# Kernel optimization log

Measured on AMD Instinct MI355X. Metric: run time of the kernel, lower is better.

Reference implementation:

```python
import jax, jax.numpy as jnp
import numpy as np

N_NODES = 50000
N_EDGES = 800000
IN_DIM = 128
HID = 128
OUT_DIM = 2


def setup_inputs() -> dict:
    key = jax.random.key(0)
    ks = jax.random.split(key, 10)
    s_in = 1.0 / np.sqrt(IN_DIM)
    s_cat = 1.0 / np.sqrt(2 * HID)
    s_h = 1.0 / np.sqrt(HID)
    return {
        "x": jax.random.normal(ks[0], (N_NODES, IN_DIM), dtype=jnp.float32),
        "edge_index": jax.random.randint(ks[1], (2, N_EDGES), 0, N_NODES, dtype=jnp.int64),
        "W_in": jax.random.uniform(ks[2], (IN_DIM, HID), jnp.float32, -s_in, s_in),
        "b_in": jnp.zeros((HID,), jnp.float32),
        "W1": jax.random.uniform(ks[3], (2 * HID, HID), jnp.float32, -s_cat, s_cat),
        "b1": jnp.zeros((HID,), jnp.float32),
        "W2": jax.random.uniform(ks[4], (HID, HID), jnp.float32, -s_h, s_h),
        "b2": jnp.zeros((HID,), jnp.float32),
        "Wc": jax.random.uniform(ks[5], (HID, OUT_DIM), jnp.float32, -s_h, s_h),
        "bc": jnp.zeros((OUT_DIM,), jnp.float32),
    }


def reference(x, edge_index, W_in, b_in, W1, b1, W2, b2, Wc, bc):
    # Input projection (eval mode: dropout is identity)
    h = jax.nn.relu(x @ W_in + b_in)                      # [N, H]
    src, dst = edge_index[0], edge_index[1]               # PyG: x_j = x[src], x_i = x[dst]
    # Per-edge message: MLP(h_i || h_j). Split the first Linear over the concat
    # halves to avoid materializing the [E, 2H] concat buffer.
    m = h[dst] @ W1[:HID] + h[src] @ W1[HID:] + b1        # [E, H]
    m = jax.nn.relu(m) @ W2 + b2                          # [E, H]
    # Scatter-add aggregation into destination nodes
    h2 = jax.ops.segment_sum(m, dst, num_segments=N_NODES)  # [N, H]
    h2 = jax.nn.relu(h2)
    return h2 @ Wc + bc                                   # [N, OUT]
```

## Files before the change

kernel.cpp:

```cpp
#include <hip/hip_runtime.h>
#include <hip/hip_bf16.h>
#include <hip/hip_fp16.h>

#define N_NODES 50000
#define N_EDGES 800000
#define HID 128
#define NPROJ 391
#define CAP 48
#define OVF_MAX 8192
#define NBIN 196
#define BINSH 8
#define BINCAP 4608
#define NCOARSE 98

typedef __bf16 bf16x8 __attribute__((ext_vector_type(8)));
typedef float f32x4 __attribute__((ext_vector_type(4)));

__global__ __launch_bounds__(256) void prep_kernel(
    const float* __restrict__ Win, const float* __restrict__ W1,
    const float* __restrict__ W2, __bf16* __restrict__ Wsw,
    int* __restrict__ curz)
{
    int id = blockIdx.x * 256 + threadIdx.x;
    int m     = id >> 14;
    int rem   = id & 16383;
    int j     = rem & 7;
    int lane  = (rem >> 3) & 63;
    int ntile = (rem >> 9) & 7;
    int kstep = rem >> 12;
    int k = kstep * 32 + (lane >> 4) * 8 + j;
    int n = ntile * 16 + (lane & 15);
    float v;
    if (m == 0)      v = Win[k * HID + n];
    else if (m == 1) v = W1[k * HID + n];
    else if (m == 2) v = W1[(k + HID) * HID + n];
    else             v = W2[k * HID + n];
    Wsw[id] = (__bf16)v;
    if (id < N_NODES + NBIN + 1) curz[id] = 0;
}

__global__ __launch_bounds__(256) void fused_kernel(
    const float* __restrict__ x, const __bf16* __restrict__ Wsw,
    const float* __restrict__ b_in, const float* __restrict__ b1,
    __half* __restrict__ P1h, __bf16* __restrict__ P1b,
    const int* __restrict__ eidx, int* __restrict__ bincnt,
    unsigned int* __restrict__ binbuf, int* __restrict__ cursor,
    int* __restrict__ ovf_cnt, uint2* __restrict__ ovf)
{
    __shared__ __bf16 At[128][136];
    int bb = blockIdx.x;
    int tid = threadIdx.x;

    if (bb < NCOARSE) {
        int* lcnt  = (int*)&At[0][0];
        int* lbase = lcnt + NBIN;
        int e0 = bb * 8192;
        for (int i = tid; i < NBIN; i += 256) lcnt[i] = 0;
        __syncthreads();
        for (int k = 0; k < 32; ++k) {
            int e = e0 + k * 256 + tid;
            if (e < N_EDGES)
                atomicAdd(&lcnt[eidx[N_EDGES + e] >> BINSH], 1);
        }
        __syncthreads();
        for (int i = tid; i < NBIN; i += 256) {
            lbase[i] = atomicAdd(&bincnt[i], lcnt[i]);
            lcnt[i] = 0;
        }
        __syncthreads();
        for (int k = 0; k < 32; ++k) {
            int e = e0 + k * 256 + tid;
            if (e < N_EDGES) {
                int d = eidx[N_EDGES + e];
                int s = eidx[e];
                int b = d >> BINSH;
                int p = lbase[b] + atomicAdd(&lcnt[b], 1);
                if (p < BINCAP) {
                    binbuf[b * BINCAP + p] = ((unsigned)d << 16) | (unsigned)s;
                } else {
                    int o = atomicAdd(ovf_cnt, 1);
                    if (o < OVF_MAX) ovf[o] = make_uint2((unsigned)d, (unsigned)s);
                    atomicAdd(&cursor[d], 1);
                }
            }
        }
        return;
    }

    int wave = tid >> 6, lane = tid & 63;
    int r_lane = lane & 15, quad = lane >> 4;
    int m0 = (bb - NCOARSE) * 128;

    for (int i = tid; i < 128 * 32; i += 256) {
        int r = i >> 5, c = i & 31;
        int row = m0 + r;
        float4 v = make_float4(0.f, 0.f, 0.f, 0.f);
        if (row < N_NODES) v = *(const float4*)(x + (long)row * HID + c * 4);
        __bf16* dst = &At[r][c * 4];
        dst[0] = (__bf16)v.x; dst[1] = (__bf16)v.y;
        dst[2] = (__bf16)v.z; dst[3] = (__bf16)v.w;
    }
    __syncthreads();

    {
        f32x4 acc[2][8] = {};
#pragma unroll
        for (int ks = 0; ks < 4; ++ks) {
            int kb = ks * 32 + quad * 8;
            bf16x8 bf[8];
#pragma unroll
            for (int n = 0; n < 8; ++n)
                bf[n] = *(const bf16x8*)(Wsw + ((ks * 8 + n) * 64 + lane) * 8);
            bf16x8 a0 = *(const bf16x8*)(&At[wave * 32 + r_lane][kb]);
            bf16x8 a1 = *(const bf16x8*)(&At[wave * 32 + 16 + r_lane][kb]);
#pragma unroll
            for (int n = 0; n < 8; ++n) {
                acc[0][n] = __builtin_amdgcn_mfma_f32_16x16x32_bf16(a0, bf[n], acc[0][n], 0, 0, 0);
                acc[1][n] = __builtin_amdgcn_mfma_f32_16x16x32_bf16(a1, bf[n], acc[1][n], 0, 0, 0);
            }
        }
#pragma unroll
        for (int n = 0; n < 8; ++n) {
            int col = n * 16 + r_lane;
            float bias = b_in[col];
#pragma unroll
            for (int mt = 0; mt < 2; ++mt) {
                int rb = wave * 32 + mt * 16 + quad * 4;
#pragma unroll
                for (int r = 0; r < 4; ++r) {
                    float v = acc[mt][n][r] + bias;
                    At[rb + r][col] = (__bf16)(v > 0.f ? v : 0.f);
                }
            }
        }
    }
    __syncthreads();

    {
        const __bf16* W1a = Wsw + 16384;
        f32x4 acc[2][8] = {};
#pragma unroll
        for (int ks = 0; ks < 4; ++ks) {
            int kb = ks * 32 + quad * 8;
            bf16x8 bf[8];
#pragma unroll
            for (int n = 0; n < 8; ++n)
                bf[n] = *(const bf16x8*)(W1a + ((ks * 8 + n) * 64 + lane) * 8);
            bf16x8 a0 = *(const bf16x8*)(&At[wave * 32 + r_lane][kb]);
            bf16x8 a1 = *(const bf16x8*)(&At[wave * 32 + 16 + r_lane][kb]);
#pragma unroll
            for (int n = 0; n < 8; ++n) {
                acc[0][n] = __builtin_amdgcn_mfma_f32_16x16x32_bf16(a0, bf[n], acc[0][n], 0, 0, 0);
                acc[1][n] = __builtin_amdgcn_mfma_f32_16x16x32_bf16(a1, bf[n], acc[1][n], 0, 0, 0);
            }
        }
#pragma unroll
        for (int n = 0; n < 8; ++n) {
            int col = n * 16 + r_lane;
            float bias = b1[col];
#pragma unroll
            for (int mt = 0; mt < 2; ++mt) {
                int rbase = m0 + wave * 32 + mt * 16 + quad * 4;
#pragma unroll
                for (int r = 0; r < 4; ++r) {
                    int row = rbase + r;
                    if (row < N_NODES)
                        P1h[(long)row * HID + col] = __float2half(acc[mt][n][r] + bias);
                }
            }
        }
    }

    {
        const __bf16* W1b = Wsw + 32768;
        f32x4 acc[2][8] = {};
#pragma unroll
        for (int ks = 0; ks < 4; ++ks) {
            int kb = ks * 32 + quad * 8;
            bf16x8 bf[8];
#pragma unroll
            for (int n = 0; n < 8; ++n)
                bf[n] = *(const bf16x8*)(W1b + ((ks * 8 + n) * 64 + lane) * 8);
            bf16x8 a0 = *(const bf16x8*)(&At[wave * 32 + r_lane][kb]);
            bf16x8 a1 = *(const bf16x8*)(&At[wave * 32 + 16 + r_lane][kb]);
#pragma unroll
            for (int n = 0; n < 8; ++n) {
                acc[0][n] = __builtin_amdgcn_mfma_f32_16x16x32_bf16(a0, bf[n], acc[0][n], 0, 0, 0);
                acc[1][n] = __builtin_amdgcn_mfma_f32_16x16x32_bf16(a1, bf[n], acc[1][n], 0, 0, 0);
            }
        }
#pragma unroll
        for (int n = 0; n < 8; ++n) {
            int col = n * 16 + r_lane;
#pragma unroll
            for (int mt = 0; mt < 2; ++mt) {
                int rbase = m0 + wave * 32 + mt * 16 + quad * 4;
#pragma unroll
                for (int r = 0; r < 4; ++r) {
                    int row = rbase + r;
                    if (row < N_NODES)
                        P1b[(long)row * HID + col] = (__bf16)acc[mt][n][r];
                }
            }
        }
    }
}

__device__ inline void acc8(float4& rA, float4& rB,
                            const float4 paA, const float4 paB, uint4 q)
{
    float t;
    t = paA.x + __uint_as_float(q.x << 16);         rA.x += t > 0.f ? t : 0.f;
    t = paA.y + __uint_as_float(q.x & 0xffff0000u); rA.y += t > 0.f ? t : 0.f;
    t = paA.z + __uint_as_float(q.y << 16);         rA.z += t > 0.f ? t : 0.f;
    t = paA.w + __uint_as_float(q.y & 0xffff0000u); rA.w += t > 0.f ? t : 0.f;
    t = paB.x + __uint_as_float(q.z << 16);         rB.x += t > 0.f ? t : 0.f;
    t = paB.y + __uint_as_float(q.z & 0xffff0000u); rB.y += t > 0.f ? t : 0.f;
    t = paB.z + __uint_as_float(q.w << 16);         rB.z += t > 0.f ? t : 0.f;
    t = paB.w + __uint_as_float(q.w & 0xffff0000u); rB.w += t > 0.f ? t : 0.f;
}

__global__ __launch_bounds__(512) void aggnode_kernel(
    const __half* __restrict__ P1h, const __bf16* __restrict__ P1b,
    const unsigned int* __restrict__ binbuf, const int* __restrict__ bincnt,
    const int* __restrict__ cursor, const int* __restrict__ ovf_cnt,
    const uint2* __restrict__ ovf, const __bf16* __restrict__ Wsw,
    const float* __restrict__ b2, const float* __restrict__ Wc,
    const float* __restrict__ bc, float* __restrict__ out)
{
    __shared__ __bf16 At[128][136];
    __shared__ unsigned short idx[128][CAP];
    __shared__ int lcur[128];
    __shared__ int degS[128];
    __shared__ unsigned int lovf[128];
    __shared__ int lovf_cnt;
    int tid = threadIdx.x;
    int blk = blockIdx.x;
    int m0 = blk * 128;
    int oc = *ovf_cnt;
    if (oc > OVF_MAX) oc = OVF_MAX;

    if (tid < 128) lcur[tid] = 0;
    if (tid == 0) lovf_cnt = 0;
    __syncthreads();
    {
        int bin = blk >> 1;
        int n = bincnt[bin];
        if (n > BINCAP) n = BINCAP;
        const unsigned int* src = binbuf + bin * BINCAP;
        for (int i = tid; i < n; i += 512) {
            unsigned int u = src[i];
            int d = (int)(u >> 16);
            if ((d >> 7) == blk) {
                int p = atomicAdd(&lcur[d & 127], 1);
                if (p < CAP) idx[d & 127][p] = (unsigned short)(u & 0xffffu);
                else { int o = atomicAdd(&lovf_cnt, 1);
                       if (o < 128) lovf[o] = u; }
            }
        }
    }
    __syncthreads();
    if (tid < 128) {
        int node = m0 + tid;
        degS[tid] = lcur[tid] + ((node < N_NODES) ? cursor[node] : 0);
    }
    __syncthreads();
    int lc = lovf_cnt;
    if (lc > 128) lc = 128;

    {
        int team = tid >> 4;
        int tl = tid & 15;
        for (int g = 0; g < 4; ++g) {
            int r = team * 4 + g;
            int node = m0 + r;
            float4 rA = make_float4(0.f, 0.f, 0.f, 0.f);
            float4 rB = make_float4(0.f, 0.f, 0.f, 0.f);
            if (node < N_NODES) {
                int deg = lcur[r];
                if (deg > CAP) deg = CAP;
                const unsigned short* ip = idx[r];
                uint4 ph = *(const uint4*)(P1h + (long)node * HID + tl * 8);
                float2 c0 = __half22float2(*(const __half2*)&ph.x);
                float2 c1 = __half22float2(*(const __half2*)&ph.y);
                float2 c2 = __half22float2(*(const __half2*)&ph.z);
                float2 c3 = __half22float2(*(const __half2*)&ph.w);
                float4 paA = make_float4(c0.x, c0.y, c1.x, c1.y);
                float4 paB = make_float4(c2.x, c2.y, c3.x, c3.y);
                int j = 0;
                for (; j + 8 <= deg; j += 8) {
                    int s0 = ip[j + 0];
                    int s1 = ip[j + 1];
                    int s2 = ip[j + 2];
                    int s3 = ip[j + 3];
                    int s4 = ip[j + 4];
                    int s5 = ip[j + 5];
                    int s6 = ip[j + 6];
                    int s7 = ip[j + 7];
                    uint4 q0 = *(const uint4*)(P1b + (long)s0 * HID + tl * 8);
                    uint4 q1 = *(const uint4*)(P1b + (long)s1 * HID + tl * 8);
                    uint4 q2 = *(const uint4*)(P1b + (long)s2 * HID + tl * 8);
                    uint4 q3 = *(const uint4*)(P1b + (long)s3 * HID + tl * 8);
                    uint4 q4 = *(const uint4*)(P1b + (long)s4 * HID + tl * 8);
                    uint4 q5 = *(const uint4*)(P1b + (long)s5 * HID + tl * 8);
                    uint4 q6 = *(const uint4*)(P1b + (long)s6 * HID + tl * 8);
                    uint4 q7 = *(const uint4*)(P1b + (long)s7 * HID + tl * 8);
                    acc8(rA, rB, paA, paB, q0);
                    acc8(rA, rB, paA, paB, q1);
                    acc8(rA, rB, paA, paB, q2);
                    acc8(rA, rB, paA, paB, q3);
                    acc8(rA, rB, paA, paB, q4);
                    acc8(rA, rB, paA, paB, q5);
                    acc8(rA, rB, paA, paB, q6);
                    acc8(rA, rB, paA, paB, q7);
                }
                for (; j < deg; ++j) {
                    int s = ip[j];
                    uint4 q = *(const uint4*)(P1b + (long)s * HID + tl * 8);
                    acc8(rA, rB, paA, paB, q);
                }
                for (int t = 0; t < lc; ++t) {
                    unsigned int u = lovf[t];
                    if ((int)(u >> 16) == node) {
                        uint4 q = *(const uint4*)(P1b + (long)(u & 0xffffu) * HID + tl * 8);
                        acc8(rA, rB, paA, paB, q);
                    }
                }
                if (oc) {
                    for (int t = 0; t < oc; ++t) {
                        uint2 e = ovf[t];
                        if ((int)e.x == node) {
                            uint4 q = *(const uint4*)(P1b + (long)e.y * HID + tl * 8);
                            acc8(rA, rB, paA, paB, q);
                        }
                    }
                }
            }
            __bf16 vv[8];
            vv[0] = (__bf16)rA.x; vv[1] = (__bf16)rA.y;
            vv[2] = (__bf16)rA.z; vv[3] = (__bf16)rA.w;
            vv[4] = (__bf16)rB.x; vv[5] = (__bf16)rB.y;
            vv[6] = (__bf16)rB.z; vv[7] = (__bf16)rB.w;
            *(uint4*)(&At[r][tl * 8]) = *(uint4*)vv;
        }
    }
    __syncthreads();

    int wave = tid >> 6, lane = tid & 63;
    int r_lane = lane & 15, quad = lane >> 4;
    const __bf16* W2f = Wsw + 49152;
    f32x4 acc[8] = {};
#pragma unroll
    for (int ks = 0; ks < 4; ++ks) {
        int kb = ks * 32 + quad * 8;
        bf16x8 bf[8];
#pragma unroll
        for (int n = 0; n < 8; ++n)
            bf[n] = *(const bf16x8*)(W2f + ((ks * 8 + n) * 64 + lane) * 8);
        bf16x8 a0 = *(const bf16x8*)(&At[wave * 16 + r_lane][kb]);
#pragma unroll
        for (int n = 0; n < 8; ++n)
            acc[n] = __builtin_amdgcn_mfma_f32_16x16x32_bf16(a0, bf[n], acc[n], 0, 0, 0);
    }

#pragma unroll
    for (int r = 0; r < 4; ++r) {
        int lr = wave * 16 + quad * 4 + r;
        int row = m0 + lr;
        float deg = (float)degS[lr];
        float s0 = 0.f, s1 = 0.f;
#pragma unroll
        for (int n = 0; n < 8; ++n) {
            int col = n * 16 + r_lane;
            float v = acc[n][r] + deg * b2[col];
            v = v > 0.f ? v : 0.f;
            s0 += v * Wc[col * 2 + 0];
            s1 += v * Wc[col * 2 + 1];
        }
#pragma unroll
        for (int off = 1; off < 16; off <<= 1) {
            s0 += __shfl_xor(s0, off);
            s1 += __shfl_xor(s1, off);
        }
        if (r_lane == 0 && row < N_NODES) {
            out[(long)row * 2 + 0] = s0 + bc[0];
            out[(long)row * 2 + 1] = s1 + bc[1];
        }
    }
}

extern "C" void kernel_launch(void* const* d_in, const int* in_sizes, int n_in,
                              void* d_out, int out_size, void* d_ws, size_t ws_size,
                              hipStream_t stream) {
    const float* x    = (const float*)d_in[0];
    const int* eidx   = (const int*)d_in[1];
    const float* W_in = (const float*)d_in[2];
    const float* b_in = (const float*)d_in[3];
    const float* W1   = (const float*)d_in[4];
    const float* b1   = (const float*)d_in[5];
    const float* W2   = (const float*)d_in[6];
    const float* b2   = (const float*)d_in[7];
    const float* Wc   = (const float*)d_in[8];
    const float* bc   = (const float*)d_in[9];
    float* out = (float*)d_out;

    char* ws = (char*)d_ws;
    __half* P1h  = (__half*)(ws + 0);
    __bf16* P1b  = (__bf16*)(ws + 12800000);
    int* cursor  = (int*)(ws + 25600000);
    int* bincnt  = cursor + N_NODES;
    int* ovf_cnt = cursor + N_NODES + NBIN;
    uint2* ovf   = (uint2*)(ws + 25800800);
    __bf16* Wsw  = (__bf16*)(ws + 25866368);
    unsigned int* binbuf = (unsigned int*)(ws + 25997440);

    prep_kernel<<<256, 256, 0, stream>>>(W_in, W1, W2, Wsw, cursor);
    fused_kernel<<<NCOARSE + NPROJ, 256, 0, stream>>>(
        x, Wsw, b_in, b1, P1h, P1b, eidx, bincnt, binbuf, cursor, ovf_cnt, ovf);
    aggnode_kernel<<<(N_NODES + 127) / 128, 512, 0, stream>>>(
        P1h, P1b, binbuf, bincnt, cursor, ovf_cnt, ovf, Wsw, b2, Wc, bc, out);
}
```

Before: 160.7 us.

## Drop prep kernel: per-block bin slots and on-the-fly weight conversion

Removes the prep kernel that pre-swizzled weights to bf16 and zeroed the global counters. Binning now writes per-(bin, coarse block) fixed slots with plain counts plus per-block overflow buffers, so no global atomics or zeroing are needed. The GEMM blocks read fp32 weights directly with strided loads and convert them to bf16 in registers. This saves a kernel launch and the global atomic contention, but adds uncoalesced weight loads in every block and a wider scan in the aggregation kernel (98×96 slots per bin plus every overflow buffer).

Result: slower. 172.5 us (+7.3%).

```diff
diff --git a/kernel.cpp b/kernel.cpp
--- a/kernel.cpp
+++ b/kernel.cpp
@@ -7,55 +7,33 @@
 #define HID 128
 #define NPROJ 391
 #define CAP 48
-#define OVF_MAX 8192
 #define NBIN 196
 #define BINSH 8
-#define BINCAP 4608
 #define NCOARSE 98
+#define CAPBB 96
+#define OVB 8192
 
 typedef __bf16 bf16x8 __attribute__((ext_vector_type(8)));
 typedef float f32x4 __attribute__((ext_vector_type(4)));
 
-__global__ __launch_bounds__(256) void prep_kernel(
-    const float* __restrict__ Win, const float* __restrict__ W1,
-    const float* __restrict__ W2, __bf16* __restrict__ Wsw,
-    int* __restrict__ curz)
-{
-    int id = blockIdx.x * 256 + threadIdx.x;
-    int m     = id >> 14;
-    int rem   = id & 16383;
-    int j     = rem & 7;
-    int lane  = (rem >> 3) & 63;
-    int ntile = (rem >> 9) & 7;
-    int kstep = rem >> 12;
-    int k = kstep * 32 + (lane >> 4) * 8 + j;
-    int n = ntile * 16 + (lane & 15);
-    float v;
-    if (m == 0)      v = Win[k * HID + n];
-    else if (m == 1) v = W1[k * HID + n];
-    else if (m == 2) v = W1[(k + HID) * HID + n];
-    else             v = W2[k * HID + n];
-    Wsw[id] = (__bf16)v;
-    if (id < N_NODES + NBIN + 1) curz[id] = 0;
-}
-
 __global__ __launch_bounds__(256) void fused_kernel(
-    const float* __restrict__ x, const __bf16* __restrict__ Wsw,
-    const float* __restrict__ b_in, const float* __restrict__ b1,
-    __half* __restrict__ P1h, __bf16* __restrict__ P1b,
-    const int* __restrict__ eidx, int* __restrict__ bincnt,
-    unsigned int* __restrict__ binbuf, int* __restrict__ cursor,
-    int* __restrict__ ovf_cnt, uint2* __restrict__ ovf)
+    const float* __restrict__ x, const float* __restrict__ Win,
+    const float* __restrict__ W1, const float* __restrict__ b_in,
+    const float* __restrict__ b1, __half* __restrict__ P1h,
+    __bf16* __restrict__ P1b, const int* __restrict__ eidx,
+    int* __restrict__ cnt2, unsigned int* __restrict__ binbuf,
+    int* __restrict__ ovfb_cnt, unsigned int* __restrict__ ovfb)
 {
     __shared__ __bf16 At[128][136];
     int bb = blockIdx.x;
     int tid = threadIdx.x;
 
     if (bb < NCOARSE) {
-        int* lcnt  = (int*)&At[0][0];
-        int* lbase = lcnt + NBIN;
+        int* lcnt = (int*)&At[0][0];
+        int* oidx = lcnt + NBIN;
         int e0 = bb * 8192;
         for (int i = tid; i < NBIN; i += 256) lcnt[i] = 0;
+        if (tid == 0) *oidx = 0;
         __syncthreads();
         for (int k = 0; k < 32; ++k) {
             int e = e0 + k * 256 + tid;
@@ -64,7 +42,7 @@
         }
         __syncthreads();
         for (int i = tid; i < NBIN; i += 256) {
-            lbase[i] = atomicAdd(&bincnt[i], lcnt[i]);
+            cnt2[i * NCOARSE + bb] = lcnt[i];
             lcnt[i] = 0;
         }
         __syncthreads();
@@ -74,16 +52,14 @@
                 int d = eidx[N_EDGES + e];
                 int s = eidx[e];
                 int b = d >> BINSH;
-                int p = lbase[b] + atomicAdd(&lcnt[b], 1);
-                if (p < BINCAP) {
-                    binbuf[b * BINCAP + p] = ((unsigned)d << 16) | (unsigned)s;
-                } else {
-                    int o = atomicAdd(ovf_cnt, 1);
-                    if (o < OVF_MAX) ovf[o] = make_uint2((unsigned)d, (unsigned)s);
-                    atomicAdd(&cursor[d], 1);
-                }
-            }
-        }
+                int p = atomicAdd(&lcnt[b], 1);
+                unsigned int u = ((unsigned)d << 16) | (unsigned)s;
+                if (p < CAPBB) binbuf[(b * NCOARSE + bb) * CAPBB + p] = u;
+                else { int o = atomicAdd(oidx, 1); ovfb[bb * OVB + o] = u; }
+            }
+        }
+        __syncthreads();
+        if (tid == 0) ovfb_cnt[bb] = *oidx;
         return;
     }
 
@@ -106,11 +82,16 @@
         f32x4 acc[2][8] = {};
 #pragma unroll
         for (int ks = 0; ks < 4; ++ks) {
+            int krow = ks * 32 + quad * 8;
+            bf16x8 bf[8];
+#pragma unroll
+            for (int n = 0; n < 8; ++n) {
+                const float* wp = Win + (long)krow * HID + n * 16 + r_lane;
+#pragma unroll
+                for (int j = 0; j < 8; ++j)
+                    bf[n][j] = (__bf16)wp[j * HID];
+            }
             int kb = ks * 32 + quad * 8;
-            bf16x8 bf[8];
-#pragma unroll
-            for (int n = 0; n < 8; ++n)
-                bf[n] = *(const bf16x8*)(Wsw + ((ks * 8 + n) * 64 + lane) * 8);
             bf16x8 a0 = *(const bf16x8*)(&At[wave * 32 + r_lane][kb]);
             bf16x8 a1 = *(const bf16x8*)(&At[wave * 32 + 16 + r_lane][kb]);
 #pragma unroll
@@ -137,15 +118,19 @@
     __syncthreads();
 
     {
-        const __bf16* W1a = Wsw + 16384;
         f32x4 acc[2][8] = {};
 #pragma unroll
         for (int ks = 0; ks < 4; ++ks) {
+            int krow = ks * 32 + quad * 8;
+            bf16x8 bf[8];
+#pragma unroll
+            for (int n = 0; n < 8; ++n) {
+                const float* wp = W1 + (long)krow * HID + n * 16 + r_lane;
+#pragma unroll
+                for (int j = 0; j < 8; ++j)
+                    bf[n][j] = (__bf16)wp[j * HID];
+            }
             int kb = ks * 32 + quad * 8;
-            bf16x8 bf[8];
-#pragma unroll
-            for (int n = 0; n < 8; ++n)
-                bf[n] = *(const bf16x8*)(W1a + ((ks * 8 + n) * 64 + lane) * 8);
             bf16x8 a0 = *(const bf16x8*)(&At[wave * 32 + r_lane][kb]);
             bf16x8 a1 = *(const bf16x8*)(&At[wave * 32 + 16 + r_lane][kb]);
 #pragma unroll
@@ -172,15 +157,20 @@
     }
 
     {
-        const __bf16* W1b = Wsw + 32768;
+        const float* W1b = W1 + (long)HID * HID;
         f32x4 acc[2][8] = {};
 #pragma unroll
         for (int ks = 0; ks < 4; ++ks) {
+            int krow = ks * 32 + quad * 8;
+            bf16x8 bf[8];
+#pragma unroll
+            for (int n = 0; n < 8; ++n) {
+                const float* wp = W1b + (long)krow * HID + n * 16 + r_lane;
+#pragma unroll
+                for (int j = 0; j < 8; ++j)
+                    bf[n][j] = (__bf16)wp[j * HID];
+            }
             int kb = ks * 32 + quad * 8;
-            bf16x8 bf[8];
-#pragma unroll
-            for (int n = 0; n < 8; ++n)
-                bf[n] = *(const bf16x8*)(W1b + ((ks * 8 + n) * 64 + lane) * 8);
             bf16x8 a0 = *(const bf16x8*)(&At[wave * 32 + r_lane][kb]);
             bf16x8 a1 = *(const bf16x8*)(&At[wave * 32 + 16 + r_lane][kb]);
 #pragma unroll
@@ -222,11 +212,11 @@
 
 __global__ __launch_bounds__(512) void aggnode_kernel(
     const __half* __restrict__ P1h, const __bf16* __restrict__ P1b,
-    const unsigned int* __restrict__ binbuf, const int* __restrict__ bincnt,
-    const int* __restrict__ cursor, const int* __restrict__ ovf_cnt,
-    const uint2* __restrict__ ovf, const __bf16* __restrict__ Wsw,
-    const float* __restrict__ b2, const float* __restrict__ Wc,
-    const float* __restrict__ bc, float* __restrict__ out)
+    const unsigned int* __restrict__ binbuf, const int* __restrict__ cnt2,
+    const int* __restrict__ ovfb_cnt, const unsigned int* __restrict__ ovfb,
+    const float* __restrict__ W2, const float* __restrict__ b2,
+    const float* __restrict__ Wc, const float* __restrict__ bc,
+    float* __restrict__ out)
 {
     __shared__ __bf16 At[128][136];
     __shared__ unsigned short idx[128][CAP];
@@ -234,36 +224,55 @@
     __shared__ int degS[128];
     __shared__ unsigned int lovf[128];
     __shared__ int lovf_cnt;
+    __shared__ int cntS[NCOARSE];
+    __shared__ int ovfS[NCOARSE];
     int tid = threadIdx.x;
     int blk = blockIdx.x;
     int m0 = blk * 128;
-    int oc = *ovf_cnt;
-    if (oc > OVF_MAX) oc = OVF_MAX;
+    int bin = blk >> 1;
 
     if (tid < 128) lcur[tid] = 0;
     if (tid == 0) lovf_cnt = 0;
+    if (tid < NCOARSE) {
+        int c = cnt2[bin * NCOARSE + tid];
+        cntS[tid] = c > CAPBB ? CAPBB : c;
+        ovfS[tid] = ovfb_cnt[tid];
+    }
     __syncthreads();
     {
-        int bin = blk >> 1;
-        int n = bincnt[bin];
-        if (n > BINCAP) n = BINCAP;
-        const unsigned int* src = binbuf + bin * BINCAP;
-        for (int i = tid; i < n; i += 512) {
-            unsigned int u = src[i];
-            int d = (int)(u >> 16);
-            if ((d >> 7) == blk) {
-                int p = atomicAdd(&lcur[d & 127], 1);
-                if (p < CAP) idx[d & 127][p] = (unsigned short)(u & 0xffffu);
-                else { int o = atomicAdd(&lovf_cnt, 1);
-                       if (o < 128) lovf[o] = u; }
-            }
-        }
-    }
-    __syncthreads();
-    if (tid < 128) {
-        int node = m0 + tid;
-        degS[tid] = lcur[tid] + ((node < N_NODES) ? cursor[node] : 0);
-    }
+        const unsigned int* base = binbuf + (long)bin * NCOARSE * CAPBB;
+        for (int i = tid; i < NCOARSE * CAPBB; i += 512) {
+            int bb2 = i / CAPBB;
+            int pos = i - bb2 * CAPBB;
+            if (pos < cntS[bb2]) {
+                unsigned int u = base[i];
+                int d = (int)(u >> 16);
+                if ((d >> 7) == blk) {
+                    int p = atomicAdd(&lcur[d & 127], 1);
+                    if (p < CAP) idx[d & 127][p] = (unsigned short)(u & 0xffffu);
+                    else { int o = atomicAdd(&lovf_cnt, 1);
+                           if (o < 128) lovf[o] = u; }
+                }
+            }
+        }
+        for (int bb2 = 0; bb2 < NCOARSE; ++bb2) {
+            int nv = ovfS[bb2];
+            if (nv <= 0) continue;
+            if (nv > OVB) nv = OVB;
+            for (int i = tid; i < nv; i += 512) {
+                unsigned int u = ovfb[bb2 * OVB + i];
+                int d = (int)(u >> 16);
+                if ((d >> 7) == blk) {
+                    int p = atomicAdd(&lcur[d & 127], 1);
+                    if (p < CAP) idx[d & 127][p] = (unsigned short)(u & 0xffffu);
+                    else { int o = atomicAdd(&lovf_cnt, 1);
+                           if (o < 128) lovf[o] = u; }
+                }
+            }
+        }
+    }
+    __syncthreads();
+    if (tid < 128) degS[tid] = lcur[tid];
     __syncthreads();
     int lc = lovf_cnt;
     if (lc > 128) lc = 128;
@@ -326,15 +335,6 @@
                         acc8(rA, rB, paA, paB, q);
                     }
                 }
-                if (oc) {
-                    for (int t = 0; t < oc; ++t) {
-                        uint2 e = ovf[t];
-                        if ((int)e.x == node) {
-                            uint4 q = *(const uint4*)(P1b + (long)e.y * HID + tl * 8);
-                            acc8(rA, rB, paA, paB, q);
-                        }
-                    }
-                }
             }
             __bf16 vv[8];
             vv[0] = (__bf16)rA.x; vv[1] = (__bf16)rA.y;
@@ -348,15 +348,19 @@
 
     int wave = tid >> 6, lane = tid & 63;
     int r_lane = lane & 15, quad = lane >> 4;
-    const __bf16* W2f = Wsw + 49152;
     f32x4 acc[8] = {};
 #pragma unroll
     for (int ks = 0; ks < 4; ++ks) {
+        int krow = ks * 32 + quad * 8;
+        bf16x8 bf[8];
+#pragma unroll
+        for (int n = 0; n < 8; ++n) {
+            const float* wp = W2 + (long)krow * HID + n * 16 + r_lane;
+#pragma unroll
+            for (int j = 0; j < 8; ++j)
+                bf[n][j] = (__bf16)wp[j * HID];
+        }
         int kb = ks * 32 + quad * 8;
-        bf16x8 bf[8];
-#pragma unroll
-        for (int n = 0; n < 8; ++n)
-            bf[n] = *(const bf16x8*)(W2f + ((ks * 8 + n) * 64 + lane) * 8);
         bf16x8 a0 = *(const bf16x8*)(&At[wave * 16 + r_lane][kb]);
 #pragma unroll
         for (int n = 0; n < 8; ++n)
@@ -407,16 +411,13 @@
     char* ws = (char*)d_ws;
     __half* P1h  = (__half*)(ws + 0);
     __bf16* P1b  = (__bf16*)(ws + 12800000);
-    int* cursor  = (int*)(ws + 25600000);
-    int* bincnt  = cursor + N_NODES;
-    int* ovf_cnt = cursor + N_NODES + NBIN;
-    uint2* ovf   = (uint2*)(ws + 25800800);
-    __bf16* Wsw  = (__bf16*)(ws + 25866368);
-    unsigned int* binbuf = (unsigned int*)(ws + 25997440);
-
-    prep_kernel<<<256, 256, 0, stream>>>(W_in, W1, W2, Wsw, cursor);
+    int* cnt2    = (int*)(ws + 25600000);
+    int* ovfb_cnt= (int*)(ws + 25676832);
+    unsigned int* binbuf = (unsigned int*)(ws + 25677312);
+    unsigned int* ovfb   = (unsigned int*)(ws + 33053184);
+
     fused_kernel<<<NCOARSE + NPROJ, 256, 0, stream>>>(
-        x, Wsw, b_in, b1, P1h, P1b, eidx, bincnt, binbuf, cursor, ovf_cnt, ovf);
+        x, W_in, W1, b_in, b1, P1h, P1b, eidx, cnt2, binbuf, ovfb_cnt, ovfb);
     aggnode_kernel<<<(N_NODES + 127) / 128, 512, 0, stream>>>(
-        P1h, P1b, binbuf, bincnt, cursor, ovf_cnt, ovf, Wsw, b2, Wc, bc, out);
+        P1h, P1b, binbuf, cnt2, ovfb_cnt, ovfb, W2, b2, Wc, bc, out);
 }
```
